# Kernel tuning notes

Hardware: AMD Instinct MI355X
Metric: run time of the kernel (lower is better)

The kernel has to match this reference:

```python
import jax, jax.numpy as jnp
import numpy as np

N = 50000
E = 500000
D_IN = 128
D_HID = 128  # hidden_channels; conv1 outputs 2*D_HID


def setup_inputs() -> dict:
    key = jax.random.key(0)
    ks = jax.random.split(key, 8)
    x = jax.random.normal(ks[0], (N, D_IN), dtype=jnp.float32)
    edge_index = jax.random.randint(ks[1], (2, E), 0, N, dtype=jnp.int64)
    # Glorot-ish init for weights, zeros for biases (PyG GCNConv default style)
    W1 = jax.random.normal(ks[2], (D_IN, 2 * D_HID), dtype=jnp.float32) / np.sqrt(D_IN)
    b1 = jnp.zeros((2 * D_HID,), dtype=jnp.float32)
    W2 = jax.random.normal(ks[3], (2 * D_HID, D_HID), dtype=jnp.float32) / np.sqrt(2 * D_HID)
    b2 = jnp.zeros((D_HID,), dtype=jnp.float32)
    Wfc = jax.random.normal(ks[4], (D_HID, 6), dtype=jnp.float32) / np.sqrt(D_HID)
    bfc = jnp.zeros((6,), dtype=jnp.float32)
    return {"x": x, "W1": W1, "b1": b1, "W2": W2, "b2": b2,
            "Wfc": Wfc, "bfc": bfc, "edge_index": edge_index}


def _gcn_conv(x, W, b, src, dst, deg_isqrt, n):
    # PyG GCNConv: h = W x; out_i = sum_j norm_ij * h_j + b, with self-loops
    h = x @ W                                  # [n, d_out]
    norm = deg_isqrt[src] * deg_isqrt[dst]     # [E+n]
    msg = h[src] * norm[:, None]               # gather + scale
    out = jax.ops.segment_sum(msg, dst, num_segments=n)  # scatter-add
    return out + b


def reference(x, W1, b1, W2, b2, Wfc, bfc, edge_index):
    n = x.shape[0]
    loop = jnp.arange(n, dtype=edge_index.dtype)
    src = jnp.concatenate([edge_index[0], loop])  # add self-loops
    dst = jnp.concatenate([edge_index[1], loop])
    deg = jax.ops.segment_sum(jnp.ones_like(dst, dtype=x.dtype), dst, num_segments=n)
    deg_isqrt = jnp.where(deg > 0, jax.lax.rsqrt(jnp.maximum(deg, 1e-12)), 0.0)
    h = jax.nn.relu(_gcn_conv(x, W1, b1, src, dst, deg_isqrt, n))
    h = jax.nn.relu(_gcn_conv(h, W2, b2, src, dst, deg_isqrt, n))
    return h @ Wfc + bfc
```

## Files before the change

### kernel.cpp

```cpp
#include <hip/hip_runtime.h>


typedef _Float16 f16;
typedef __attribute__((ext_vector_type(8))) _Float16 f16x8;
typedef __attribute__((ext_vector_type(4))) float f32x4;

#define GLOAD16(g, l)                                                      \
    __builtin_amdgcn_global_load_lds(                                      \
        (const __attribute__((address_space(1))) void*)(g),                \
        (__attribute__((address_space(3))) void*)(l), 16, 0, 0)

__global__ void count_kernel(const int* __restrict__ dst, int* __restrict__ cnt,
                             int e) {
    for (int i = blockIdx.x * blockDim.x + threadIdx.x; i < e;
         i += gridDim.x * blockDim.x)
        atomicAdd(&cnt[dst[i]], 1);
}

__global__ void scan1_kernel(const int* __restrict__ cnt, int* __restrict__ local,
                             int* __restrict__ partials, float* __restrict__ disq,
                             int n) {
    __shared__ int lds[256];
    int base = blockIdx.x * 1024;
    int t = threadIdx.x;
    int v[4];
    int sum = 0;
    #pragma unroll
    for (int j = 0; j < 4; j++) {
        int i = base + t * 4 + j;
        v[j] = (i < n) ? cnt[i] : 0;
        if (i < n) disq[i] = rsqrtf(1.0f + (float)v[j]);
        sum += v[j];
    }
    lds[t] = sum;
    __syncthreads();
    for (int off = 1; off < 256; off <<= 1) {
        int x = (t >= off) ? lds[t - off] : 0;
        __syncthreads();
        lds[t] += x;
        __syncthreads();
    }
    int excl = lds[t] - sum;
    if (t == 255) partials[blockIdx.x] = lds[255];
    int run = excl;
    #pragma unroll
    for (int j = 0; j < 4; j++) {
        int i = base + t * 4 + j;
        if (i < n) local[i] = run;
        run += v[j];
    }
}

__global__ void scan2_kernel(int* __restrict__ partials, int nb) {
    __shared__ int lds[1024];
    int t = threadIdx.x;
    int v = (t < nb) ? partials[t] : 0;
    lds[t] = v;
    __syncthreads();
    for (int off = 1; off < 1024; off <<= 1) {
        int x = (t >= off) ? lds[t - off] : 0;
        __syncthreads();
        lds[t] += x;
        __syncthreads();
    }
    if (t < nb) partials[t] = lds[t] - v;
}

__global__ void scan3_kernel(const int* __restrict__ local,
                             const int* __restrict__ partials,
                             int* __restrict__ row_ptr, int* __restrict__ cursor,
                             int n, int e_total) {
    int base = blockIdx.x * 1024;
    int add = partials[blockIdx.x];
    int t = threadIdx.x;
    #pragma unroll
    for (int j = 0; j < 4; j++) {
        int i = base + t * 4 + j;
        if (i < n) {
            int p = local[i] + add;
            row_ptr[i] = p;
            cursor[i] = p;
        }
    }
    if (blockIdx.x == 0 && t == 0) row_ptr[n] = e_total;
}

__global__ void csr_fill_kernel(const int* __restrict__ src, const int* __restrict__ dst,
                                int* __restrict__ cursor, int* __restrict__ esorted,
                                int e) {
    for (int i = blockIdx.x * blockDim.x + threadIdx.x; i < e;
         i += gridDim.x * blockDim.x) {
        int d = dst[i];
        int pos = atomicAdd(&cursor[d], 1);
        esorted[pos] = src[i];
    }
}

__global__ void cvt_all_kernel(const float4* __restrict__ x,
                               const float* __restrict__ disq,
                               f16* __restrict__ xs,
                               const float* __restrict__ W1, f16* __restrict__ wt1,
                               const float* __restrict__ W2, f16* __restrict__ wt2,
                               long long n4) {
    long long i = blockIdx.x * (long long)blockDim.x + threadIdx.x;
    if (i < n4) {
        float4 v = x[i];
        float s = disq[i >> 5];
        union { f16 h[4]; short4 s4; } u;
        u.h[0] = (f16)(v.x * s); u.h[1] = (f16)(v.y * s);
        u.h[2] = (f16)(v.z * s); u.h[3] = (f16)(v.w * s);
        *(short4*)(xs + i * 4) = u.s4;
        return;
    }
    long long j = i - n4;
    if (j < 32768) {
        int nn = (int)(j >> 7), k = (int)(j & 127);
        wt1[j] = (f16)W1[(long long)k * 256 + nn];
        return;
    }
    j -= 32768;
    if (j < 32768) {
        int nn = (int)(j >> 8), k = (int)(j & 255);
        wt2[j] = (f16)W2[(long long)k * 128 + nn];
    }
}

template <int MODE>
__global__ __launch_bounds__(256)
void gemm_f16_kernel(const f16* __restrict__ A,
                     const f16* __restrict__ Bt,
                     f16* __restrict__ C,
                     const float* __restrict__ rowscale,
                     const float* __restrict__ bias,
                     int M, int K, int Nc) {
    __shared__ __align__(16) char smem[2 * 24 * 1024];
    const int tid = threadIdx.x;
    const int lane = tid & 63;
    const int wid = tid >> 6;
    const int wr = wid >> 1;
    const int wc = wid & 1;
    const int row0 = blockIdx.y * 128;
    const int col0 = blockIdx.x * 64;
    const bool rows_full = (row0 + 128 <= M);

    f32x4 acc[4][2];
    #pragma unroll
    for (int mr = 0; mr < 4; mr++)
        #pragma unroll
        for (int nr = 0; nr < 2; nr++)
            acc[mr][nr] = (f32x4){0.f, 0.f, 0.f, 0.f};

    auto stage = [&](int buf, int k0) {
        char* as = smem + buf * (24 * 1024);
        char* bs = as + 16 * 1024;
        if (rows_full) {
            #pragma unroll
            for (int i = 0; i < 4; i++) {
                int flat = i * 256 + tid;
                int r = flat >> 3, gp = flat & 7;
                int g = gp ^ (r & 7);
                const f16* src = A + (long long)(row0 + r) * K + k0 + g * 8;
                GLOAD16(src, as + (i * 256 + wid * 64) * 16);
            }
        } else {
            #pragma unroll
            for (int i = 0; i < 4; i++) {
                int flat = i * 256 + tid;
                int r = flat >> 3, gp = flat & 7;
                int g = gp ^ (r & 7);
                int gr = row0 + r;
                float4 v = {0.f, 0.f, 0.f, 0.f};
                if (gr < M) v = *(const float4*)(A + (long long)gr * K + k0 + g * 8);
                *(float4*)(as + flat * 16) = v;
            }
        }
        #pragma unroll
        for (int i = 0; i < 2; i++) {
            int flat = i * 256 + tid;
            int nn = flat >> 3, gp = flat & 7;
            int g = gp ^ (nn & 7);
            const f16* src = Bt + (long long)(col0 + nn) * K + k0 + g * 8;
            GLOAD16(src, bs + (i * 256 + wid * 64) * 16);
        }
    };

    auto compute = [&](int buf) {
        char* as = smem + buf * (24 * 1024);
        char* bs = as + 16 * 1024;
        #pragma unroll
        for (int ks = 0; ks < 2; ks++) {
            const int kb = (ks * 32 + ((lane >> 4) * 8)) * 2;
            f16x8 af[4], bf[2];
            #pragma unroll
            for (int mr = 0; mr < 4; mr++) {
                int r = wr * 64 + mr * 16 + (lane & 15);
                af[mr] = *(const f16x8*)(as + r * 128 + (kb ^ ((r & 7) << 4)));
            }
            #pragma unroll
            for (int nr = 0; nr < 2; nr++) {
                int c = wc * 32 + nr * 16 + (lane & 15);
                bf[nr] = *(const f16x8*)(bs + c * 128 + (kb ^ ((c & 7) << 4)));
            }
            #pragma unroll
            for (int mr = 0; mr < 4; mr++)
                #pragma unroll
                for (int nr = 0; nr < 2; nr++)
                    acc[mr][nr] = __builtin_amdgcn_mfma_f32_16x16x32_f16(
                        af[mr], bf[nr], acc[mr][nr], 0, 0, 0);
        }
    };

    const int nt = K >> 6;
    stage(0, 0);
    __syncthreads();
    int cur = 0;
    for (int t = 0; t < nt; t++) {
        if (t + 1 < nt) stage(cur ^ 1, (t + 1) * 64);
        compute(cur);
        __syncthreads();
        cur ^= 1;
    }

    float bv[2] = {0.f, 0.f};
    if (MODE == 1) {
        #pragma unroll
        for (int nr = 0; nr < 2; nr++)
            bv[nr] = bias[col0 + wc * 32 + nr * 16 + (lane & 15)];
    }
    #pragma unroll
    for (int mr = 0; mr < 4; mr++) {
        #pragma unroll
        for (int reg = 0; reg < 4; reg++) {
            int row = row0 + wr * 64 + mr * 16 + (lane >> 4) * 4 + reg;
            if (row < M) {
                float s = rowscale[row];
                int col = col0 + wc * 32 + (lane & 15);
                #pragma unroll
                for (int nr = 0; nr < 2; nr++) {
                    float v = acc[mr][nr][reg] * s;
                    if (MODE == 1) v = fmaxf(v + bv[nr], 0.0f);
                    C[(long long)row * Nc + col + nr * 16] = (f16)v;
                }
            }
        }
    }
}

__global__ void gather_sum_f16_kernel(const float4* __restrict__ h,
                                      float4* __restrict__ out,
                                      const int* __restrict__ row_ptr,
                                      const int* __restrict__ esorted, int n) {
    int lane = threadIdx.x & 63;
    long long wave = (blockIdx.x * (long long)blockDim.x + threadIdx.x) >> 6;
    int sub = lane >> 4;
    int sl = lane & 15;
    long long node = wave * 4 + sub;
    if (node >= n) return;
    int beg = row_ptr[node], end = row_ptr[node + 1];
    float acc[8];
    {
        float4 v = h[node * 16 + sl];
        const f16* hp = (const f16*)&v;
        #pragma unroll
        for (int j = 0; j < 8; j++) acc[j] = (float)hp[j];
    }
    int e = beg;
    for (; e + 4 <= end; e += 4) {
        int s0 = esorted[e], s1 = esorted[e + 1];
        int s2 = esorted[e + 2], s3 = esorted[e + 3];
        float4 v0 = h[(long long)s0 * 16 + sl];
        float4 v1 = h[(long long)s1 * 16 + sl];
        float4 v2 = h[(long long)s2 * 16 + sl];
        float4 v3 = h[(long long)s3 * 16 + sl];
        const f16 *p0 = (const f16*)&v0, *p1 = (const f16*)&v1;
        const f16 *p2 = (const f16*)&v2, *p3 = (const f16*)&v3;
        #pragma unroll
        for (int j = 0; j < 8; j++)
            acc[j] += (float)p0[j] + (float)p1[j] + (float)p2[j] + (float)p3[j];
    }
    for (; e < end; e++) {
        int s = esorted[e];
        float4 v = h[(long long)s * 16 + sl];
        const f16* hp = (const f16*)&v;
        #pragma unroll
        for (int j = 0; j < 8; j++) acc[j] += (float)hp[j];
    }
    union { float4 f4; f16 hh[8]; } o;
    #pragma unroll
    for (int j = 0; j < 8; j++) o.hh[j] = (f16)acc[j];
    out[node * 16 + sl] = o.f4;
}

__global__ void gather_fc_kernel(const float4* __restrict__ t,
                                 const int* __restrict__ row_ptr,
                                 const int* __restrict__ esorted,
                                 const float* __restrict__ disq,
                                 const float* __restrict__ b2,
                                 const float* __restrict__ Wfc,
                                 const float* __restrict__ bfc,
                                 float* __restrict__ out, int n) {
    __shared__ float wf[6 * 132];
    for (int i = threadIdx.x; i < 6 * 128; i += 256) {
        int k = i >> 7, ch = i & 127;
        wf[k * 132 + ch] = Wfc[ch * 6 + k];
    }
    __syncthreads();
    int lane = threadIdx.x & 63;
    long long wave = (blockIdx.x * (long long)blockDim.x + threadIdx.x) >> 6;
    int sub = lane >> 4;
    int sl = lane & 15;
    long long node = wave * 4 + sub;
    if (node >= n) return;
    int beg = row_ptr[node], end = row_ptr[node + 1];
    float acc[8];
    {
        float4 v = t[node * 16 + sl];
        const f16* hp = (const f16*)&v;
        #pragma unroll
        for (int j = 0; j < 8; j++) acc[j] = (float)hp[j];
    }
    int e = beg;
    for (; e + 4 <= end; e += 4) {
        int s0 = esorted[e], s1 = esorted[e + 1];
        int s2 = esorted[e + 2], s3 = esorted[e + 3];
        float4 v0 = t[(long long)s0 * 16 + sl];
        float4 v1 = t[(long long)s1 * 16 + sl];
        float4 v2 = t[(long long)s2 * 16 + sl];
        float4 v3 = t[(long long)s3 * 16 + sl];
        const f16 *p0 = (const f16*)&v0, *p1 = (const f16*)&v1;
        const f16 *p2 = (const f16*)&v2, *p3 = (const f16*)&v3;
        #pragma unroll
        for (int j = 0; j < 8; j++)
            acc[j] += (float)p0[j] + (float)p1[j] + (float)p2[j] + (float)p3[j];
    }
    for (; e < end; e++) {
        int s = esorted[e];
        float4 v = t[(long long)s * 16 + sl];
        const f16* hp = (const f16*)&v;
        #pragma unroll
        for (int j = 0; j < 8; j++) acc[j] += (float)hp[j];
    }
    float sc = disq[node];
    const float4* b4 = (const float4*)(b2 + sl * 8);
    float4 bb0 = b4[0], bb1 = b4[1];
    float bb[8] = {bb0.x, bb0.y, bb0.z, bb0.w, bb1.x, bb1.y, bb1.z, bb1.w};
    float h2[8];
    #pragma unroll
    for (int j = 0; j < 8; j++)
        h2[j] = fmaxf(fmaf(acc[j], sc, bb[j]), 0.0f);
    float p[6];
    #pragma unroll
    for (int k = 0; k < 6; k++) {
        float s = 0.f;
        #pragma unroll
        for (int j = 0; j < 8; j++) s += h2[j] * wf[k * 132 + sl * 8 + j];
        p[k] = s;
    }
    #pragma unroll
    for (int off = 8; off >= 1; off >>= 1)
        #pragma unroll
        for (int k = 0; k < 6; k++) p[k] += __shfl_down(p[k], off);
    if (sl == 0) {
        #pragma unroll
        for (int k = 0; k < 6; k++)
            out[(long long)node * 6 + k] = p[k] + bfc[k];
    }
}

extern "C" void kernel_launch(void* const* d_in, const int* in_sizes, int n_in,
                              void* d_out, int out_size, void* d_ws, size_t ws_size,
                              hipStream_t stream) {
    const float* x   = (const float*)d_in[0];
    const float* W1  = (const float*)d_in[1];
    const float* b1  = (const float*)d_in[2];
    const float* W2  = (const float*)d_in[3];
    const float* b2  = (const float*)d_in[4];
    const float* Wfc = (const float*)d_in[5];
    const float* bfc = (const float*)d_in[6];
    const int* edges = (const int*)d_in[7];

    const int N = in_sizes[0] / 128;
    const int E = in_sizes[7] / 2;
    const int* e_src = edges;
    const int* e_dst = edges + E;

    char* ws = (char*)d_ws;
    size_t off = 0;
    auto alloc = [&](size_t bytes) {
        void* p = ws + off;
        off += (bytes + 255) & ~(size_t)255;
        return p;
    };
    const int NB = (N + 1023) / 1024;
    float* disq     = (float*)alloc((size_t)N * 4);
    int*   cnt      = (int*)  alloc((size_t)N * 4);
    int*   slocal   = (int*)  alloc((size_t)N * 4);
    int*   partials = (int*)  alloc((size_t)NB * 4);
    int*   row_ptr  = (int*)  alloc((size_t)(N + 1) * 4);
    int*   cursor   = (int*)  alloc((size_t)N * 4);
    int*   esorted  = (int*)  alloc((size_t)E * 4);
    f16*   xs       = (f16*)  alloc((size_t)N * 128 * 2);
    f16*   wt1      = (f16*)  alloc((size_t)256 * 128 * 2);
    f16*   wt2      = (f16*)  alloc((size_t)128 * 256 * 2);
    f16*   agg1     = (f16*)  alloc((size_t)N * 128 * 2);
    f16*   h1       = (f16*)  alloc((size_t)N * 256 * 2);
    f16*   tbuf     = (f16*)  alloc((size_t)N * 128 * 2);
    (void)ws_size; (void)n_in;

    float* out = (float*)d_out; (void)out_size;

    hipMemsetAsync(cnt, 0, (size_t)N * sizeof(int), stream);
    count_kernel<<<2048, 256, 0, stream>>>(e_dst, cnt, E);
    scan1_kernel<<<NB, 256, 0, stream>>>(cnt, slocal, partials, disq, N);
    scan2_kernel<<<1, 1024, 0, stream>>>(partials, NB);
    scan3_kernel<<<NB, 256, 0, stream>>>(slocal, partials, row_ptr, cursor, N, E);
    csr_fill_kernel<<<2048, 256, 0, stream>>>(e_src, e_dst, cursor, esorted, E);

    {
        long long n4 = (long long)N * 128 / 4;
        long long total = n4 + 32768 + 32768;
        cvt_all_kernel<<<(int)((total + 255) / 256), 256, 0, stream>>>(
            (const float4*)x, disq, xs, W1, wt1, W2, wt2, n4);
    }

    {
        long long waves = ((long long)N + 3) / 4;
        int blocks = (int)((waves + 3) / 4);
        gather_sum_f16_kernel<<<blocks, 256, 0, stream>>>(
            (const float4*)xs, (float4*)agg1, row_ptr, esorted, N);
    }
    {
        dim3 g(256 / 64, (N + 127) / 128);
        gemm_f16_kernel<1><<<g, 256, 0, stream>>>(agg1, wt1, h1, disq, b1,
                                                  N, 128, 256);
    }

    {
        dim3 g(128 / 64, (N + 127) / 128);
        gemm_f16_kernel<0><<<g, 256, 0, stream>>>(h1, wt2, tbuf, disq, nullptr,
                                                  N, 256, 128);
    }
    {
        long long waves = ((long long)N + 3) / 4;
        int blocks = (int)((waves + 3) / 4);
        gather_fc_kernel<<<blocks, 256, 0, stream>>>(
            (const float4*)tbuf, row_ptr, esorted, disq, b2, Wfc, bfc, out, N);
    }
}
```

Baseline: 234.8 us.

## Fuse preprocessing kernels, widen GEMM tile to 128 columns, unroll gathers by eight

The weight-transpose conversion moves into the degree-count kernel and the x scaling/conversion moves into the scan3 kernel, which removes one launch and overlaps independent work. The GEMM block tile grows from 128x64 to 128x128, so A tiles are reloaded fewer times, at the cost of more LDS and accumulator registers per block. The gather loops now issue eight independent row loads per iteration instead of four, giving more memory-level parallelism but using more registers.

```diff
diff --git a/kernel.cpp b/kernel.cpp
--- a/kernel.cpp
+++ b/kernel.cpp
@@ -10,11 +10,23 @@
         (const __attribute__((address_space(1))) void*)(g),                \
         (__attribute__((address_space(3))) void*)(l), 16, 0, 0)
 
-__global__ void count_kernel(const int* __restrict__ dst, int* __restrict__ cnt,
-                             int e) {
-    for (int i = blockIdx.x * blockDim.x + threadIdx.x; i < e;
-         i += gridDim.x * blockDim.x)
-        atomicAdd(&cnt[dst[i]], 1);
+__global__ void count_wt_kernel(const int* __restrict__ dst, int* __restrict__ cnt,
+                                int e,
+                                const float* __restrict__ W1, f16* __restrict__ wt1,
+                                const float* __restrict__ W2, f16* __restrict__ wt2) {
+    int b = blockIdx.x;
+    if (b < 128) {
+        int j = b * 256 + threadIdx.x;
+        int nn = j >> 7, k = j & 127;
+        wt1[j] = (f16)W1[(long long)k * 256 + nn];
+    } else if (b < 256) {
+        int j = (b - 128) * 256 + threadIdx.x;
+        int nn = j >> 8, k = j & 255;
+        wt2[j] = (f16)W2[(long long)k * 128 + nn];
+    } else {
+        for (int i = (b - 256) * 256 + (int)threadIdx.x; i < e; i += 2048 * 256)
+            atomicAdd(&cnt[dst[i]], 1);
+    }
 }
 
 __global__ void scan1_kernel(const int* __restrict__ cnt, int* __restrict__ local,
@@ -66,23 +78,39 @@
     if (t < nb) partials[t] = lds[t] - v;
 }
 
-__global__ void scan3_kernel(const int* __restrict__ local,
-                             const int* __restrict__ partials,
-                             int* __restrict__ row_ptr, int* __restrict__ cursor,
-                             int n, int e_total) {
-    int base = blockIdx.x * 1024;
-    int add = partials[blockIdx.x];
+__global__ void scan3_xs_kernel(const int* __restrict__ local,
+                                const int* __restrict__ partials,
+                                int* __restrict__ row_ptr, int* __restrict__ cursor,
+                                int n, int e_total, int nb,
+                                const float4* __restrict__ x,
+                                const float* __restrict__ disq,
+                                f16* __restrict__ xs, long long n4) {
+    int b = blockIdx.x;
     int t = threadIdx.x;
-    #pragma unroll
-    for (int j = 0; j < 4; j++) {
-        int i = base + t * 4 + j;
-        if (i < n) {
-            int p = local[i] + add;
-            row_ptr[i] = p;
-            cursor[i] = p;
-        }
-    }
-    if (blockIdx.x == 0 && t == 0) row_ptr[n] = e_total;
+    if (b < nb) {
+        int base = b * 1024;
+        int add = partials[b];
+        #pragma unroll
+        for (int j = 0; j < 4; j++) {
+            int i = base + t * 4 + j;
+            if (i < n) {
+                int p = local[i] + add;
+                row_ptr[i] = p;
+                cursor[i] = p;
+            }
+        }
+        if (b == 0 && t == 0) row_ptr[n] = e_total;
+        return;
+    }
+    long long i = (long long)(b - nb) * 256 + t;
+    if (i < n4) {
+        float4 v = x[i];
+        float s = disq[i >> 5];
+        union { f16 h[4]; short4 s4; } u;
+        u.h[0] = (f16)(v.x * s); u.h[1] = (f16)(v.y * s);
+        u.h[2] = (f16)(v.z * s); u.h[3] = (f16)(v.w * s);
+        *(short4*)(xs + i * 4) = u.s4;
+    }
 }
 
 __global__ void csr_fill_kernel(const int* __restrict__ src, const int* __restrict__ dst,
@@ -96,35 +124,6 @@
     }
 }
 
-__global__ void cvt_all_kernel(const float4* __restrict__ x,
-                               const float* __restrict__ disq,
-                               f16* __restrict__ xs,
-                               const float* __restrict__ W1, f16* __restrict__ wt1,
-                               const float* __restrict__ W2, f16* __restrict__ wt2,
-                               long long n4) {
-    long long i = blockIdx.x * (long long)blockDim.x + threadIdx.x;
-    if (i < n4) {
-        float4 v = x[i];
-        float s = disq[i >> 5];
-        union { f16 h[4]; short4 s4; } u;
-        u.h[0] = (f16)(v.x * s); u.h[1] = (f16)(v.y * s);
-        u.h[2] = (f16)(v.z * s); u.h[3] = (f16)(v.w * s);
-        *(short4*)(xs + i * 4) = u.s4;
-        return;
-    }
-    long long j = i - n4;
-    if (j < 32768) {
-        int nn = (int)(j >> 7), k = (int)(j & 127);
-        wt1[j] = (f16)W1[(long long)k * 256 + nn];
-        return;
-    }
-    j -= 32768;
-    if (j < 32768) {
-        int nn = (int)(j >> 8), k = (int)(j & 255);
-        wt2[j] = (f16)W2[(long long)k * 128 + nn];
-    }
-}
-
 template <int MODE>
 __global__ __launch_bounds__(256)
 void gemm_f16_kernel(const f16* __restrict__ A,
@@ -133,25 +132,25 @@
                      const float* __restrict__ rowscale,
                      const float* __restrict__ bias,
                      int M, int K, int Nc) {
-    __shared__ __align__(16) char smem[2 * 24 * 1024];
+    __shared__ __align__(16) char smem[2 * 32 * 1024];
     const int tid = threadIdx.x;
     const int lane = tid & 63;
     const int wid = tid >> 6;
     const int wr = wid >> 1;
     const int wc = wid & 1;
     const int row0 = blockIdx.y * 128;
-    const int col0 = blockIdx.x * 64;
+    const int col0 = blockIdx.x * 128;
     const bool rows_full = (row0 + 128 <= M);
 
-    f32x4 acc[4][2];
+    f32x4 acc[4][4];
     #pragma unroll
     for (int mr = 0; mr < 4; mr++)
         #pragma unroll
-        for (int nr = 0; nr < 2; nr++)
+        for (int nr = 0; nr < 4; nr++)
             acc[mr][nr] = (f32x4){0.f, 0.f, 0.f, 0.f};
 
     auto stage = [&](int buf, int k0) {
-        char* as = smem + buf * (24 * 1024);
+        char* as = smem + buf * (32 * 1024);
         char* bs = as + 16 * 1024;
         if (rows_full) {
             #pragma unroll
@@ -175,7 +174,7 @@
             }
         }
         #pragma unroll
-        for (int i = 0; i < 2; i++) {
+        for (int i = 0; i < 4; i++) {
             int flat = i * 256 + tid;
             int nn = flat >> 3, gp = flat & 7;
             int g = gp ^ (nn & 7);
@@ -185,26 +184,26 @@
     };
 
     auto compute = [&](int buf) {
-        char* as = smem + buf * (24 * 1024);
+        char* as = smem + buf * (32 * 1024);
         char* bs = as + 16 * 1024;
         #pragma unroll
         for (int ks = 0; ks < 2; ks++) {
             const int kb = (ks * 32 + ((lane >> 4) * 8)) * 2;
-            f16x8 af[4], bf[2];
+            f16x8 af[4], bf[4];
             #pragma unroll
             for (int mr = 0; mr < 4; mr++) {
                 int r = wr * 64 + mr * 16 + (lane & 15);
                 af[mr] = *(const f16x8*)(as + r * 128 + (kb ^ ((r & 7) << 4)));
             }
             #pragma unroll
-            for (int nr = 0; nr < 2; nr++) {
-                int c = wc * 32 + nr * 16 + (lane & 15);
+            for (int nr = 0; nr < 4; nr++) {
+                int c = wc * 64 + nr * 16 + (lane & 15);
                 bf[nr] = *(const f16x8*)(bs + c * 128 + (kb ^ ((c & 7) << 4)));
             }
             #pragma unroll
             for (int mr = 0; mr < 4; mr++)
                 #pragma unroll
-                for (int nr = 0; nr < 2; nr++)
+                for (int nr = 0; nr < 4; nr++)
                     acc[mr][nr] = __builtin_amdgcn_mfma_f32_16x16x32_f16(
                         af[mr], bf[nr], acc[mr][nr], 0, 0, 0);
         }
@@ -221,11 +220,11 @@
         cur ^= 1;
     }
 
-    float bv[2] = {0.f, 0.f};
+    float bv[4] = {0.f, 0.f, 0.f, 0.f};
     if (MODE == 1) {
         #pragma unroll
-        for (int nr = 0; nr < 2; nr++)
-            bv[nr] = bias[col0 + wc * 32 + nr * 16 + (lane & 15)];
+        for (int nr = 0; nr < 4; nr++)
+            bv[nr] = bias[col0 + wc * 64 + nr * 16 + (lane & 15)];
     }
     #pragma unroll
     for (int mr = 0; mr < 4; mr++) {
@@ -234,9 +233,9 @@
             int row = row0 + wr * 64 + mr * 16 + (lane >> 4) * 4 + reg;
             if (row < M) {
                 float s = rowscale[row];
-                int col = col0 + wc * 32 + (lane & 15);
+                int col = col0 + wc * 64 + (lane & 15);
                 #pragma unroll
-                for (int nr = 0; nr < 2; nr++) {
+                for (int nr = 0; nr < 4; nr++) {
                     float v = acc[mr][nr][reg] * s;
                     if (MODE == 1) v = fmaxf(v + bv[nr], 0.0f);
                     C[(long long)row * Nc + col + nr * 16] = (f16)v;
@@ -265,18 +264,19 @@
         for (int j = 0; j < 8; j++) acc[j] = (float)hp[j];
     }
     int e = beg;
-    for (; e + 4 <= end; e += 4) {
-        int s0 = esorted[e], s1 = esorted[e + 1];
-        int s2 = esorted[e + 2], s3 = esorted[e + 3];
-        float4 v0 = h[(long long)s0 * 16 + sl];
-        float4 v1 = h[(long long)s1 * 16 + sl];
-        float4 v2 = h[(long long)s2 * 16 + sl];
-        float4 v3 = h[(long long)s3 * 16 + sl];
-        const f16 *p0 = (const f16*)&v0, *p1 = (const f16*)&v1;
-        const f16 *p2 = (const f16*)&v2, *p3 = (const f16*)&v3;
-        #pragma unroll
-        for (int j = 0; j < 8; j++)
-            acc[j] += (float)p0[j] + (float)p1[j] + (float)p2[j] + (float)p3[j];
+    for (; e + 8 <= end; e += 8) {
+        int s[8];
+        #pragma unroll
+        for (int u = 0; u < 8; u++) s[u] = esorted[e + u];
+        float4 v[8];
+        #pragma unroll
+        for (int u = 0; u < 8; u++) v[u] = h[(long long)s[u] * 16 + sl];
+        #pragma unroll
+        for (int u = 0; u < 8; u++) {
+            const f16* p = (const f16*)&v[u];
+            #pragma unroll
+            for (int j = 0; j < 8; j++) acc[j] += (float)p[j];
+        }
     }
     for (; e < end; e++) {
         int s = esorted[e];
@@ -320,18 +320,19 @@
         for (int j = 0; j < 8; j++) acc[j] = (float)hp[j];
     }
     int e = beg;
-    for (; e + 4 <= end; e += 4) {
-        int s0 = esorted[e], s1 = esorted[e + 1];
-        int s2 = esorted[e + 2], s3 = esorted[e + 3];
-        float4 v0 = t[(long long)s0 * 16 + sl];
-        float4 v1 = t[(long long)s1 * 16 + sl];
-        float4 v2 = t[(long long)s2 * 16 + sl];
-        float4 v3 = t[(long long)s3 * 16 + sl];
-        const f16 *p0 = (const f16*)&v0, *p1 = (const f16*)&v1;
-        const f16 *p2 = (const f16*)&v2, *p3 = (const f16*)&v3;
-        #pragma unroll
-        for (int j = 0; j < 8; j++)
-            acc[j] += (float)p0[j] + (float)p1[j] + (float)p2[j] + (float)p3[j];
+    for (; e + 8 <= end; e += 8) {
+        int s[8];
+        #pragma unroll
+        for (int u = 0; u < 8; u++) s[u] = esorted[e + u];
+        float4 v[8];
+        #pragma unroll
+        for (int u = 0; u < 8; u++) v[u] = t[(long long)s[u] * 16 + sl];
+        #pragma unroll
+        for (int u = 0; u < 8; u++) {
+            const f16* p = (const f16*)&v[u];
+            #pragma unroll
+            for (int j = 0; j < 8; j++) acc[j] += (float)p[j];
+        }
     }
     for (; e < end; e++) {
         int s = esorted[e];
@@ -410,18 +411,18 @@
     float* out = (float*)d_out; (void)out_size;
 
     hipMemsetAsync(cnt, 0, (size_t)N * sizeof(int), stream);
-    count_kernel<<<2048, 256, 0, stream>>>(e_dst, cnt, E);
+    count_wt_kernel<<<256 + 2048, 256, 0, stream>>>(e_dst, cnt, E,
+                                                    W1, wt1, W2, wt2);
     scan1_kernel<<<NB, 256, 0, stream>>>(cnt, slocal, partials, disq, N);
     scan2_kernel<<<1, 1024, 0, stream>>>(partials, NB);
-    scan3_kernel<<<NB, 256, 0, stream>>>(slocal, partials, row_ptr, cursor, N, E);
+    {
+        long long n4 = (long long)N * 128 / 4;
+        int xb = (int)((n4 + 255) / 256);
+        scan3_xs_kernel<<<NB + xb, 256, 0, stream>>>(
+            slocal, partials, row_ptr, cursor, N, E, NB,
+            (const float4*)x, disq, xs, n4);
+    }
     csr_fill_kernel<<<2048, 256, 0, stream>>>(e_src, e_dst, cursor, esorted, E);
-
-    {
-        long long n4 = (long long)N * 128 / 4;
-        long long total = n4 + 32768 + 32768;
-        cvt_all_kernel<<<(int)((total + 255) / 256), 256, 0, stream>>>(
-            (const float4*)x, disq, xs, W1, wt1, W2, wt2, n4);
-    }
 
     {
         long long waves = ((long long)N + 3) / 4;
@@ -430,13 +431,13 @@
             (const float4*)xs, (float4*)agg1, row_ptr, esorted, N);
     }
     {
-        dim3 g(256 / 64, (N + 127) / 128);
+        dim3 g(256 / 128, (N + 127) / 128);
         gemm_f16_kernel<1><<<g, 256, 0, stream>>>(agg1, wt1, h1, disq, b1,
                                                   N, 128, 256);
     }
 
     {
-        dim3 g(128 / 64, (N + 127) / 128);
+        dim3 g(128 / 128, (N + 127) / 128);
         gemm_f16_kernel<0><<<g, 256, 0, stream>>>(h1, wt2, tbuf, disq, nullptr,
                                                   N, 256, 128);
     }
```

Measured after the change: 229.1 us. 2.5% less time.
